# Kernel tuning notes

Hardware: AMD Instinct MI355X
Metric: run time of the kernel (lower is better)

## Reference

```python
import jax, jax.numpy as jnp
import numpy as np

DIM = 384
WS = 8        # window_size
SHIFT = 4     # shift_size
HEADS = 8
HEAD_DIM = DIM // HEADS
SCALE = HEAD_DIM ** (-0.5)
EPS = 1e-5


def layernorm(x, g, b):
    m = jnp.mean(x, axis=-1, keepdims=True)
    v = jnp.var(x, axis=-1, keepdims=True)
    return (x - m) * jax.lax.rsqrt(v + EPS) * g + b


def setup_inputs() -> dict:
    key = jax.random.key(0)
    ks = jax.random.split(key, 8)
    s = 0.02
    return {
        "x": jax.random.normal(ks[0], (8, DIM, 64, 64), dtype=jnp.float32),
        "qkv_w": jax.random.normal(ks[1], (DIM, 3 * DIM), dtype=jnp.float32) * s,
        "qkv_b": jnp.zeros((3 * DIM,), jnp.float32),
        "proj_w": jax.random.normal(ks[2], (DIM, DIM), dtype=jnp.float32) * s,
        "proj_b": jnp.zeros((DIM,), jnp.float32),
        "ln1_g": jnp.ones((DIM,), jnp.float32),
        "ln1_b": jnp.zeros((DIM,), jnp.float32),
        "ln2_g": jnp.ones((DIM,), jnp.float32),
        "ln2_b": jnp.zeros((DIM,), jnp.float32),
        "mlp_w1": jax.random.normal(ks[3], (DIM, 4 * DIM), dtype=jnp.float32) * s,
        "mlp_b1": jnp.zeros((4 * DIM,), jnp.float32),
        "mlp_w2": jax.random.normal(ks[4], (4 * DIM, DIM), dtype=jnp.float32) * s,
        "mlp_b2": jnp.zeros((DIM,), jnp.float32),
    }


def reference(x, qkv_w, qkv_b, proj_w, proj_b, ln1_g, ln1_b, ln2_g, ln2_b,
              mlp_w1, mlp_b1, mlp_w2, mlp_b2):
    B, C, H, W = x.shape
    x_skip = jnp.transpose(x, (0, 2, 3, 1))  # [B,H,W,C]
    xh = x_skip
    pad_b = (-H) % WS
    pad_r = (-W) % WS
    xh = jnp.pad(xh, ((0, 0), (0, pad_b), (0, pad_r), (0, 0)))
    Hp, Wp = xh.shape[1], xh.shape[2]
    if SHIFT > 0:
        xh = jnp.roll(xh, (-SHIFT, -SHIFT), axis=(1, 2))
    # window partition -> [B*nH*nW, WS*WS, C]
    win = xh.reshape(B, Hp // WS, WS, Wp // WS, WS, C)
    win = win.transpose(0, 1, 3, 2, 4, 5).reshape(-1, WS * WS, C)
    win = layernorm(win, ln1_g, ln1_b)
    # windowed MHA (no shift mask in original module)
    Bw, N, _ = win.shape
    qkv = (win @ qkv_w + qkv_b).reshape(Bw, N, 3, HEADS, HEAD_DIM)
    qkv = qkv.transpose(2, 0, 3, 1, 4)  # [3, Bw, H, N, d]
    q, k, v = qkv[0] * SCALE, qkv[1], qkv[2]
    attn = jax.nn.softmax(jnp.einsum('bhnd,bhmd->bhnm', q, k), axis=-1)
    out = jnp.einsum('bhnm,bhmd->bhnd', attn, v)
    out = out.transpose(0, 2, 1, 3).reshape(Bw, N, C)
    out = out @ proj_w + proj_b
    # window reverse
    xh = out.reshape(B, Hp // WS, Wp // WS, WS, WS, C)
    xh = xh.transpose(0, 1, 3, 2, 4, 5).reshape(B, Hp, Wp, C)
    if SHIFT > 0:
        xh = jnp.roll(xh, (SHIFT, SHIFT), axis=(1, 2))
    xh = xh[:, :H, :W, :] + x_skip
    h = layernorm(xh, ln2_g, ln2_b)
    h = jax.nn.gelu(h @ mlp_w1 + mlp_b1, approximate=False) @ mlp_w2 + mlp_b2
    return jnp.transpose(h, (0, 3, 1, 2))  # [B,C,H,W]
```

## Files before the change

### kernel.cpp

```cpp
#include <hip/hip_runtime.h>
#include <hip/hip_bf16.h>
#include <math.h>

#define DIM   384
#define HEADS 8
#define HD    48
#define NTOK  32768
#define NWIN  512

typedef __attribute__((ext_vector_type(8))) short bf16x8;
typedef __attribute__((ext_vector_type(8))) unsigned short u16x8;
typedef __attribute__((ext_vector_type(4))) float f32x4;

__device__ __forceinline__ float bf2f(unsigned short u) {
    unsigned int v = ((unsigned int)u) << 16;
    return __uint_as_float(v);
}
__device__ __forceinline__ unsigned short f2bf(float f) {
    __bf16 b = (__bf16)f;
    return __builtin_bit_cast(unsigned short, b);
}

__device__ __forceinline__ float gelu(float v) {
    float z  = v * 0.70710678118654752f;
    float az = fabsf(z);
    float t  = __builtin_amdgcn_rcpf(1.0f + 0.47047f * az);
    float p  = t * (0.3480242f + t * (-0.0958798f + t * 0.7478556f));
    float ea = 1.0f - p * __expf(-az * az);
    float er = copysignf(ea, z);
    return 0.5f * v * (1.0f + er);
}

__device__ __forceinline__ void tok2src(int tok, int& b, int& hs, int& ws) {
    int bb  = tok >> 12;
    int win = (tok >> 6) & 63;
    int t   = tok & 63;
    int hi = win >> 3, wi = win & 7;
    int r  = t >> 3,  cc = t & 7;
    b  = bb;
    hs = (hi * 8 + r  + 4) & 63;
    ws = (wi * 8 + cc + 4) & 63;
}

__global__ __launch_bounds__(256) void k_wt4(const float* __restrict__ qkv_w,
                                             const float* __restrict__ proj_w,
                                             const float* __restrict__ w1,
                                             const float* __restrict__ w2,
                                             unsigned short* __restrict__ d0,
                                             unsigned short* __restrict__ d1,
                                             unsigned short* __restrict__ d2,
                                             unsigned short* __restrict__ d3) {
    __shared__ unsigned short T[64][66];
    int b = blockIdx.x;
    const float* W; unsigned short* Wt; int K, N, lt;
    if (b < 108)      { W = qkv_w;  Wt = d0; K = 384;  N = 1152; lt = b; }
    else if (b < 144) { W = proj_w; Wt = d1; K = 384;  N = 384;  lt = b - 108; }
    else if (b < 288) { W = w1;     Wt = d2; K = 384;  N = 1536; lt = b - 144; }
    else              { W = w2;     Wt = d3; K = 1536; N = 384;  lt = b - 288; }
    int tn = N >> 6;
    int k0 = (lt / tn) << 6, n0 = (lt % tn) << 6;
    int t  = threadIdx.x;
    int cl = t & 63, rw = t >> 6;
    #pragma unroll
    for (int p = 0; p < 16; p++) {
        int kk = p * 4 + rw;
        T[cl][kk] = f2bf(W[(size_t)(k0 + kk) * N + n0 + cl]);
    }
    __syncthreads();
    #pragma unroll
    for (int p = 0; p < 16; p++) {
        int nn = p * 4 + rw;
        Wt[(size_t)(n0 + nn) * K + k0 + cl] = T[nn][cl];
    }
}

__global__ __launch_bounds__(256) void k_ln1(const float* __restrict__ x,
                                             const float* __restrict__ g,
                                             const float* __restrict__ bt,
                                             unsigned short* __restrict__ ln1) {
    int blk = blockIdx.x;
    int b  = blk >> 6, hs = blk & 63;
    int t  = threadIdx.x;
    int w  = t & 63, cg = t >> 6;
    const float* row = x + (size_t)b * DIM * 4096 + hs * 64;

    float v[96];
    float sum = 0.f, sq = 0.f;
    #pragma unroll
    for (int i = 0; i < 96; i++) {
        int c = i * 4 + cg;
        float xv = row[(size_t)c * 4096 + w];
        v[i] = xv;
        sum += xv; sq += xv * xv;
    }
    __shared__ float red[2][4][64];
    __shared__ float mean_s[64], rstd_s[64];
    red[0][cg][w] = sum; red[1][cg][w] = sq;
    __syncthreads();
    if (t < 64) {
        float s  = red[0][0][t] + red[0][1][t] + red[0][2][t] + red[0][3][t];
        float q2 = red[1][0][t] + red[1][1][t] + red[1][2][t] + red[1][3][t];
        float mean = s * (1.0f / DIM);
        float var  = q2 * (1.0f / DIM) - mean * mean;
        mean_s[t] = mean;
        rstd_s[t] = rsqrtf(var + 1e-5f);
    }
    __syncthreads();

    int wp = t >> 2, seg = t & 3;
    int hr = (hs + 60) & 63, wr = (wp + 60) & 63;
    int tok = ((b * 8 + (hr >> 3)) * 8 + (wr >> 3)) * 64 + (hr & 7) * 8 + (wr & 7);

    __shared__ __align__(16) unsigned short tile[64][72];
    #pragma unroll
    for (int chunk = 0; chunk < 6; chunk++) {
        float mean = mean_s[w], rstd = rstd_s[w];
        #pragma unroll
        for (int it = 0; it < 16; it++) {
            int cl = it * 4 + cg;
            int c  = chunk * 64 + cl;
            tile[w][cl] = f2bf((v[chunk * 16 + it] - mean) * rstd * g[c] + bt[c]);
        }
        __syncthreads();
        u16x8 v0 = *(const u16x8*)&tile[wp][seg * 16];
        u16x8 v1 = *(const u16x8*)&tile[wp][seg * 16 + 8];
        unsigned short* op = ln1 + (size_t)tok * DIM + chunk * 64 + seg * 16;
        *(u16x8*)op = v0;
        *(u16x8*)(op + 8) = v1;
        __syncthreads();
    }
}

template <int EPI, int K>
__global__ __launch_bounds__(256) void k_gemm_mfma(
        const unsigned short* __restrict__ A,
        const unsigned short* __restrict__ Bt,
        const float* __restrict__ bias,
        void* __restrict__ Cout,
        const float* __restrict__ xres,
        int N, int GX) {
    __shared__ __align__(16) unsigned short SH[24576];
    int tid  = threadIdx.x;
    int lane = tid & 63;
    int wave = tid >> 6;
    int wm = wave >> 1, wn = wave & 1;
    int quad = lane >> 4, l15 = lane & 15;

    int l   = blockIdx.x;
    int xcd = l & 7;
    int r_  = l >> 3;
    int bx  = r_ % GX;
    int by  = (r_ / GX) * 8 + xcd;
    int m0 = by * 128, n0 = bx * 128;

    const unsigned short* gA0 = A  + (size_t)(m0 +      lane) * K + wave * 8;
    const unsigned short* gA1 = A  + (size_t)(m0 + 64 + lane) * K + wave * 8;
    const unsigned short* gB0 = Bt + (size_t)(n0 +      lane) * K + wave * 8;
    const unsigned short* gB1 = Bt + (size_t)(n0 + 64 + lane) * K + wave * 8;

    auto stage = [&](int buf) {
        __builtin_amdgcn_global_load_lds(
            (const __attribute__((address_space(1))) void*)gA0,
            (__attribute__((address_space(3))) void*)&SH[buf * 4096 + wave * 1024],
            16, 0, 0);
        __builtin_amdgcn_global_load_lds(
            (const __attribute__((address_space(1))) void*)gA1,
            (__attribute__((address_space(3))) void*)&SH[buf * 4096 + wave * 1024 + 512],
            16, 0, 0);
        __builtin_amdgcn_global_load_lds(
            (const __attribute__((address_space(1))) void*)gB0,
            (__attribute__((address_space(3))) void*)&SH[12288 + buf * 4096 + wave * 1024],
            16, 0, 0);
        __builtin_amdgcn_global_load_lds(
            (const __attribute__((address_space(1))) void*)gB1,
            (__attribute__((address_space(3))) void*)&SH[12288 + buf * 4096 + wave * 1024 + 512],
            16, 0, 0);
        gA0 += 32; gA1 += 32; gB0 += 32; gB1 += 32;
    };

    f32x4 acc[4][4] = {};
    constexpr int NSTEPS = K >> 5;
    constexpr int U = NSTEPS / 3;

    int oa = (quad * 128 + wm * 64 + l15) * 8;
    int ob = 12288 + (quad * 128 + wn * 64 + l15) * 8;

    stage(0);
    stage(1);

#define GSTEP(CUR, NXT, MODE)                                                \
    {                                                                        \
        __builtin_amdgcn_s_barrier();                                        \
        if constexpr ((MODE) == 0) {                                         \
            stage(NXT);                                                      \
            asm volatile("s_waitcnt vmcnt(8)" ::: "memory");                 \
        } else if constexpr ((MODE) == 1) {                                  \
            asm volatile("s_waitcnt vmcnt(4)" ::: "memory");                 \
        } else {                                                             \
            asm volatile("s_waitcnt vmcnt(0)" ::: "memory");                 \
        }                                                                    \
        __builtin_amdgcn_s_barrier();                                        \
        bf16x8 af[4], bfr[4];                                                \
        _Pragma("unroll")                                                    \
        for (int r = 0; r < 4; r++)                                          \
            af[r] = *(const bf16x8*)&SH[(CUR) * 4096 + oa + r * 128];        \
        _Pragma("unroll")                                                    \
        for (int r2 = 0; r2 < 4; r2++)                                       \
            bfr[r2] = *(const bf16x8*)&SH[(CUR) * 4096 + ob + r2 * 128];     \
        _Pragma("unroll")                                                    \
        for (int r = 0; r < 4; r++)                                          \
            _Pragma("unroll")                                                \
            for (int r2 = 0; r2 < 4; r2++)                                   \
                acc[r][r2] = __builtin_amdgcn_mfma_f32_16x16x32_bf16(        \
                                 af[r], bfr[r2], acc[r][r2], 0, 0, 0);       \
    }

    #pragma unroll 1
    for (int u = 0; u < U - 1; ++u) {
        GSTEP(0, 2, 0)
        GSTEP(1, 0, 0)
        GSTEP(2, 1, 0)
    }
    GSTEP(0, 2, 0)
    GSTEP(1, 0, 1)
    GSTEP(2, 0, 2)
#undef GSTEP

    if constexpr (EPI == 3) {
        #pragma unroll
        for (int r2 = 0; r2 < 4; r2++) {
            int n = n0 + wn * 64 + r2 * 16 + l15;
            float bn = bias[n];
            #pragma unroll
            for (int r = 0; r < 4; r++) {
                #pragma unroll
                for (int reg = 0; reg < 4; reg++) {
                    int m = m0 + wm * 64 + r * 16 + quad * 4 + reg;
                    ((float*)Cout)[(size_t)m * N + n] = acc[r][r2][reg] + bn;
                }
            }
        }
    } else if constexpr (EPI == 5) {
        float* SF = (float*)SH;
        __syncthreads();
        int b   = m0 >> 12;
        int hs0 = (m0 >> 6) & 63;
        #pragma unroll
        for (int h2 = 0; h2 < 2; h2++) {
            if (wm == h2) {
                #pragma unroll
                for (int r2 = 0; r2 < 4; r2++) {
                    int c = wn * 64 + r2 * 16 + l15;
                    float bn = bias[n0 + c];
                    #pragma unroll
                    for (int r = 0; r < 4; r++) {
                        f32x4 v4;
                        #pragma unroll
                        for (int reg = 0; reg < 4; reg++)
                            v4[reg] = acc[r][r2][reg] + bn;
                        *(f32x4*)&SF[c * 68 + r * 16 + quad * 4] = v4;
                    }
                }
            }
            __syncthreads();
            #pragma unroll
            for (int i = 0; i < 8; i++) {
                int id = tid + i * 256;
                int c  = id >> 4, ch = id & 15;
                f32x4 v = *(const f32x4*)&SF[c * 68 + ch * 4];
                float* dst = (float*)Cout + ((size_t)(b * DIM + n0 + c) * 64 + hs0 + h2) * 64;
                *(f32x4*)&dst[ch * 4] = v;
            }
            __syncthreads();
        }
    } else {
        __syncthreads();
        #pragma unroll
        for (int r2 = 0; r2 < 4; r2++) {
            int col = wn * 64 + r2 * 16 + l15;
            float bn = bias[n0 + col];
            #pragma unroll
            for (int r = 0; r < 4; r++) {
                int row0 = wm * 64 + r * 16 + quad * 4;
                #pragma unroll
                for (int reg = 0; reg < 4; reg++) {
                    int row = row0 + reg;
                    float v = acc[r][r2][reg] + bn;
                    if (EPI == 1) v = gelu(v);
                    SH[(row * 136 + col) ^ (((row >> 3) & 1) << 4)] = f2bf(v);
                }
            }
        }
        __syncthreads();
        #pragma unroll
        for (int i = 0; i < 8; i++) {
            int chunk = tid + i * 256;
            int m = chunk >> 4, nc = chunk & 15;
            int idx = (m * 136 + nc * 8) ^ (((m >> 3) & 1) << 4);
            u16x8 v = *(const u16x8*)&SH[idx];
            if (EPI == 4) {
                int n = n0 + nc * 8;
                int qi  = n / 384;
                int rem = n - qi * 384;
                int hh  = rem / 48;
                int d   = rem - hh * 48;
                *(u16x8*)&((unsigned short*)Cout)[((size_t)(qi * 8 + hh) * NTOK + m0 + m) * 48 + d] = v;
            } else {
                *(u16x8*)&((unsigned short*)Cout)[(size_t)(m0 + m) * N + n0 + nc * 8] = v;
            }
        }
    }
}

__global__ __launch_bounds__(256, 1) void k_fused(
        const unsigned short* __restrict__ qkvh,
        const unsigned short* __restrict__ proj_wt,
        const float* __restrict__ proj_b,
        const float* __restrict__ x,
        const float* __restrict__ ln2_g,
        const float* __restrict__ ln2_b,
        unsigned short* __restrict__ out) {
    __shared__ __align__(16) unsigned short lds[4][8064];
    __shared__ __align__(16) unsigned short AT[64][392];
    __shared__ float red[2][4][64];
    __shared__ float mrs[2][64];
    int tid  = threadIdx.x;
    int lane = tid & 63;
    int wave = tid >> 6;
    int quad = lane >> 4, l15 = lane & 15;
    int win  = blockIdx.x;
    int tok0 = win * 64;
    unsigned short* VT = &lds[wave][0];
    unsigned short* P  = &lds[wave][3456];
    const float scale = 0.14433756729740643f;

    for (int hi = 0; hi < 2; hi++) {
        int h = wave + hi * 4;
        const unsigned short* qb = qkvh + ((size_t)(0 * 8 + h) * NTOK + tok0) * 48;
        const unsigned short* kb = qkvh + ((size_t)(1 * 8 + h) * NTOK + tok0) * 48;
        const unsigned short* vb = qkvh + ((size_t)(2 * 8 + h) * NTOK + tok0) * 48;

        #pragma unroll
        for (int i = 0; i < 6; i++) {
            u16x8 v = *(const u16x8*)&vb[lane * 48 + i * 8];
            #pragma unroll
            for (int j = 0; j < 8; j++)
                VT[(i * 8 + j) * 72 + lane] = v[j];
        }

        bf16x8 kf[4][2];
        #pragma unroll
        for (int ni = 0; ni < 4; ni++) {
            kf[ni][0] = *(const bf16x8*)&kb[(ni * 16 + l15) * 48 + quad * 8];
            bf16x8 z = {};
            if (quad < 2)
                z = *(const bf16x8*)&kb[(ni * 16 + l15) * 48 + 32 + quad * 8];
            kf[ni][1] = z;
        }

        f32x4 sacc[4][4] = {};
        #pragma unroll
        for (int mi = 0; mi < 4; mi++) {
            bf16x8 qf0 = *(const bf16x8*)&qb[(mi * 16 + l15) * 48 + quad * 8];
            bf16x8 qf1 = {};
            if (quad < 2)
                qf1 = *(const bf16x8*)&qb[(mi * 16 + l15) * 48 + 32 + quad * 8];
            #pragma unroll
            for (int ni = 0; ni < 4; ni++) {
                sacc[mi][ni] = __builtin_amdgcn_mfma_f32_16x16x32_bf16(qf0, kf[ni][0], sacc[mi][ni], 0, 0, 0);
                sacc[mi][ni] = __builtin_amdgcn_mfma_f32_16x16x32_bf16(qf1, kf[ni][1], sacc[mi][ni], 0, 0, 0);
            }
        }

        #pragma unroll
        for (int mi = 0; mi < 4; mi++) {
            #pragma unroll
            for (int reg = 0; reg < 4; reg++) {
                float s0 = sacc[mi][0][reg] * scale;
                float s1 = sacc[mi][1][reg] * scale;
                float s2 = sacc[mi][2][reg] * scale;
                float s3 = sacc[mi][3][reg] * scale;
                float mx = fmaxf(fmaxf(s0, s1), fmaxf(s2, s3));
                #pragma unroll
                for (int off = 1; off < 16; off <<= 1)
                    mx = fmaxf(mx, __shfl_xor(mx, off));
                float e0 = __expf(s0 - mx);
                float e1 = __expf(s1 - mx);
                float e2 = __expf(s2 - mx);
                float e3 = __expf(s3 - mx);
                float sm = e0 + e1 + e2 + e3;
                #pragma unroll
                for (int off = 1; off < 16; off <<= 1)
                    sm += __shfl_xor(sm, off);
                float inv = 1.0f / sm;
                int row = mi * 16 + quad * 4 + reg;
                P[row * 72 +  0 + l15] = f2bf(e0 * inv);
                P[row * 72 + 16 + l15] = f2bf(e1 * inv);
                P[row * 72 + 32 + l15] = f2bf(e2 * inv);
                P[row * 72 + 48 + l15] = f2bf(e3 * inv);
            }
        }

        bf16x8 vf[3][2];
        #pragma unroll
        for (int ni = 0; ni < 3; ni++)
            #pragma unroll
            for (int kt = 0; kt < 2; kt++)
                vf[ni][kt] = *(const bf16x8*)&VT[(ni * 16 + l15) * 72 + kt * 32 + quad * 8];

        #pragma unroll
        for (int mi = 0; mi < 4; mi++) {
            bf16x8 pf0 = *(const bf16x8*)&P[(mi * 16 + l15) * 72 + quad * 8];
            bf16x8 pf1 = *(const bf16x8*)&P[(mi * 16 + l15) * 72 + 32 + quad * 8];
            f32x4 o[3] = {};
            #pragma unroll
            for (int ni = 0; ni < 3; ni++) {
                o[ni] = __builtin_amdgcn_mfma_f32_16x16x32_bf16(pf0, vf[ni][0], o[ni], 0, 0, 0);
                o[ni] = __builtin_amdgcn_mfma_f32_16x16x32_bf16(pf1, vf[ni][1], o[ni], 0, 0, 0);
            }
            #pragma unroll
            for (int ni = 0; ni < 3; ni++)
                #pragma unroll
                for (int reg = 0; reg < 4; reg++)
                    AT[mi * 16 + quad * 4 + reg][h * HD + ni * 16 + l15] = f2bf(o[ni][reg]);
        }
    }
    __syncthreads();

    f32x4 pacc[4][6] = {};
    const unsigned short* Bw = proj_wt + (size_t)(wave * 96) * 384;
    bf16x8 bcur[6], bnxt[6];
    #pragma unroll
    for (int nj = 0; nj < 6; nj++)
        bcur[nj] = *(const bf16x8*)&Bw[(nj * 16 + l15) * 384 + quad * 8];
    #pragma unroll 1
    for (int ks = 0; ks < 12; ++ks) {
        if (ks + 1 < 12) {
            #pragma unroll
            for (int nj = 0; nj < 6; nj++)
                bnxt[nj] = *(const bf16x8*)&Bw[(nj * 16 + l15) * 384 + (ks + 1) * 32 + quad * 8];
        }
        bf16x8 a[4];
        #pragma unroll
        for (int mi = 0; mi < 4; mi++)
            a[mi] = *(const bf16x8*)&AT[mi * 16 + l15][ks * 32 + quad * 8];
        #pragma unroll
        for (int mi = 0; mi < 4; mi++)
            #pragma unroll
            for (int nj = 0; nj < 6; nj++)
                pacc[mi][nj] = __builtin_amdgcn_mfma_f32_16x16x32_bf16(
                                   a[mi], bcur[nj], pacc[mi][nj], 0, 0, 0);
        #pragma unroll
        for (int nj = 0; nj < 6; nj++) bcur[nj] = bnxt[nj];
    }

    #pragma unroll
    for (int mi = 0; mi < 4; mi++) {
        #pragma unroll
        for (int reg = 0; reg < 4; reg++) {
            int tok = tok0 + mi * 16 + quad * 4 + reg;
            int b, hs, ws_;
            tok2src(tok, b, hs, ws_);
            const float* xr = x + (((size_t)b * DIM) * 64 + hs) * 64 + ws_;
            #pragma unroll
            for (int nj = 0; nj < 6; nj++) {
                int c = wave * 96 + nj * 16 + l15;
                pacc[mi][nj][reg] += proj_b[c] + xr[(size_t)c * 4096];
            }
        }
    }

    #pragma unroll
    for (int mi = 0; mi < 4; mi++) {
        #pragma unroll
        for (int reg = 0; reg < 4; reg++) {
            float s = 0.f, q = 0.f;
            #pragma unroll
            for (int nj = 0; nj < 6; nj++) {
                float v = pacc[mi][nj][reg];
                s += v; q += v * v;
            }
            #pragma unroll
            for (int off = 1; off < 16; off <<= 1) {
                s += __shfl_xor(s, off);
                q += __shfl_xor(q, off);
            }
            if (l15 == 0) {
                int row = mi * 16 + quad * 4 + reg;
                red[0][wave][row] = s;
                red[1][wave][row] = q;
            }
        }
    }
    __syncthreads();
    if (tid < 64) {
        float s = red[0][0][tid] + red[0][1][tid] + red[0][2][tid] + red[0][3][tid];
        float q = red[1][0][tid] + red[1][1][tid] + red[1][2][tid] + red[1][3][tid];
        float mean = s * (1.0f / DIM);
        float var  = q * (1.0f / DIM) - mean * mean;
        mrs[0][tid] = mean;
        mrs[1][tid] = rsqrtf(var + 1e-5f);
    }
    __syncthreads();

    #pragma unroll
    for (int mi = 0; mi < 4; mi++) {
        #pragma unroll
        for (int nj = 0; nj < 6; nj++) {
            int c = wave * 96 + nj * 16 + l15;
            float gg = ln2_g[c], bb = ln2_b[c];
            #pragma unroll
            for (int reg = 0; reg < 4; reg++) {
                int row = mi * 16 + quad * 4 + reg;
                float v = (pacc[mi][nj][reg] - mrs[0][row]) * mrs[1][row] * gg + bb;
                AT[row][c] = f2bf(v);
            }
        }
    }
    __syncthreads();
    #pragma unroll
    for (int i = 0; i < 12; i++) {
        int id  = tid + i * 256;
        int row = id / 48, ch = id - row * 48;
        int b, hs, ws_;
        tok2src(tok0 + row, b, hs, ws_);
        int p = (b * 64 + hs) * 64 + ws_;
        u16x8 v = *(const u16x8*)&AT[row][ch * 8];
        *(u16x8*)&out[(size_t)p * DIM + ch * 8] = v;
    }
}

extern "C" void kernel_launch(void* const* d_in, const int* in_sizes, int n_in,
                              void* d_out, int out_size, void* d_ws, size_t ws_size,
                              hipStream_t stream) {
    const float* x      = (const float*)d_in[0];
    const float* qkv_w  = (const float*)d_in[1];
    const float* qkv_b  = (const float*)d_in[2];
    const float* proj_w = (const float*)d_in[3];
    const float* proj_b = (const float*)d_in[4];
    const float* ln1_g  = (const float*)d_in[5];
    const float* ln1_b  = (const float*)d_in[6];
    const float* ln2_g  = (const float*)d_in[7];
    const float* ln2_b  = (const float*)d_in[8];
    const float* w1     = (const float*)d_in[9];
    const float* b1     = (const float*)d_in[10];
    const float* w2     = (const float*)d_in[11];
    const float* b2     = (const float*)d_in[12];

    char* ws = (char*)d_ws;
    unsigned short* qkv_wt  = (unsigned short*)(ws + 0);
    unsigned short* proj_wt = (unsigned short*)(ws + 884736);
    unsigned short* w1t     = (unsigned short*)(ws + 1179648);
    unsigned short* w2t     = (unsigned short*)(ws + 2359296);
    unsigned short* ln1     = (unsigned short*)(ws + 4194304);
    unsigned short* qkv     = (unsigned short*)(ws + 29360128);
    unsigned short* ln2     = ln1;
    unsigned short* mid     = qkv;

    k_wt4<<<432, 256, 0, stream>>>(qkv_w, proj_w, w1, w2, qkv_wt, proj_wt, w1t, w2t);
    k_ln1<<<512, 256, 0, stream>>>(x, ln1_g, ln1_b, ln1);
    k_gemm_mfma<4, 384><<<9 * 256, 256, 0, stream>>>(ln1, qkv_wt, qkv_b, qkv, nullptr, 1152, 9);
    k_fused<<<NWIN, 256, 0, stream>>>(qkv, proj_wt, proj_b, x, ln2_g, ln2_b, ln2);
    k_gemm_mfma<1, 384><<<12 * 256, 256, 0, stream>>>(ln2, w1t, b1, mid, nullptr, 1536, 12);
    k_gemm_mfma<5, 1536><<<3 * 256, 256, 0, stream>>>(mid, w2t, b2, (float*)d_out, nullptr, 384, 3);
}
```

Before: 441.2 us.

## Prefetch V and residual loads, deepen proj weight prefetch, add MFMA priority

In the attention+projection kernel, the V tile for the second head is now prefetched into registers while the first head is processed. The residual x values are loaded as float4 vectors before the projection GEMM, replacing scalar strided loads after it. The proj weight prefetch is deepened to two k-steps with the loop fully unrolled, and s_setprio is raised around the MFMA blocks. The aim is to hide global memory latency behind compute, at the cost of considerably more register pressure (xres alone is 96 floats), which may reduce occupancy or cause spills.

```diff
diff --git a/kernel.cpp b/kernel.cpp
--- a/kernel.cpp
+++ b/kernel.cpp
@@ -334,18 +334,29 @@
     unsigned short* P  = &lds[wave][3456];
     const float scale = 0.14433756729740643f;
 
+    const unsigned short* vb1g = qkvh + ((size_t)(2 * 8 + wave + 4) * NTOK + tok0) * 48;
+    u16x8 vpre[6];
+    {
+        const unsigned short* vb0g = qkvh + ((size_t)(2 * 8 + wave) * NTOK + tok0) * 48;
+        #pragma unroll
+        for (int i = 0; i < 6; i++)
+            vpre[i] = *(const u16x8*)&vb0g[lane * 48 + i * 8];
+    }
+    #pragma unroll
     for (int hi = 0; hi < 2; hi++) {
         int h = wave + hi * 4;
         const unsigned short* qb = qkvh + ((size_t)(0 * 8 + h) * NTOK + tok0) * 48;
         const unsigned short* kb = qkvh + ((size_t)(1 * 8 + h) * NTOK + tok0) * 48;
-        const unsigned short* vb = qkvh + ((size_t)(2 * 8 + h) * NTOK + tok0) * 48;
-
-        #pragma unroll
-        for (int i = 0; i < 6; i++) {
-            u16x8 v = *(const u16x8*)&vb[lane * 48 + i * 8];
+
+        #pragma unroll
+        for (int i = 0; i < 6; i++)
             #pragma unroll
             for (int j = 0; j < 8; j++)
-                VT[(i * 8 + j) * 72 + lane] = v[j];
+                VT[(i * 8 + j) * 72 + lane] = vpre[i][j];
+        if (hi == 0) {
+            #pragma unroll
+            for (int i = 0; i < 6; i++)
+                vpre[i] = *(const u16x8*)&vb1g[lane * 48 + i * 8];
         }
 
         bf16x8 kf[4][2];
@@ -365,11 +376,13 @@
             bf16x8 qf1 = {};
             if (quad < 2)
                 qf1 = *(const bf16x8*)&qb[(mi * 16 + l15) * 48 + 32 + quad * 8];
+            __builtin_amdgcn_s_setprio(1);
             #pragma unroll
             for (int ni = 0; ni < 4; ni++) {
                 sacc[mi][ni] = __builtin_amdgcn_mfma_f32_16x16x32_bf16(qf0, kf[ni][0], sacc[mi][ni], 0, 0, 0);
                 sacc[mi][ni] = __builtin_amdgcn_mfma_f32_16x16x32_bf16(qf1, kf[ni][1], sacc[mi][ni], 0, 0, 0);
             }
+            __builtin_amdgcn_s_setprio(0);
         }
 
         #pragma unroll
@@ -413,11 +426,13 @@
             bf16x8 pf0 = *(const bf16x8*)&P[(mi * 16 + l15) * 72 + quad * 8];
             bf16x8 pf1 = *(const bf16x8*)&P[(mi * 16 + l15) * 72 + 32 + quad * 8];
             f32x4 o[3] = {};
+            __builtin_amdgcn_s_setprio(1);
             #pragma unroll
             for (int ni = 0; ni < 3; ni++) {
                 o[ni] = __builtin_amdgcn_mfma_f32_16x16x32_bf16(pf0, vf[ni][0], o[ni], 0, 0, 0);
                 o[ni] = __builtin_amdgcn_mfma_f32_16x16x32_bf16(pf1, vf[ni][1], o[ni], 0, 0, 0);
             }
+            __builtin_amdgcn_s_setprio(0);
             #pragma unroll
             for (int ni = 0; ni < 3; ni++)
                 #pragma unroll
@@ -427,48 +442,62 @@
     }
     __syncthreads();
 
+    int bimg = win >> 6;
+    int hi_i = (win >> 3) & 7, wi_i = win & 7;
+    int ws0  = (wi_i * 8 + ((quad & 1) << 2) + 4) & 63;
+    f32x4 xres[4][6];
+    #pragma unroll
+    for (int mi = 0; mi < 4; mi++) {
+        int hs_ = (hi_i * 8 + mi * 2 + (quad >> 1) + 4) & 63;
+        #pragma unroll
+        for (int nj = 0; nj < 6; nj++) {
+            int c = wave * 96 + nj * 16 + l15;
+            xres[mi][nj] = *(const f32x4*)&x[((size_t)(bimg * DIM + c) * 64 + hs_) * 64 + ws0];
+        }
+    }
+
     f32x4 pacc[4][6] = {};
     const unsigned short* Bw = proj_wt + (size_t)(wave * 96) * 384;
-    bf16x8 bcur[6], bnxt[6];
+    bf16x8 bk0[6], bk1[6];
     #pragma unroll
     for (int nj = 0; nj < 6; nj++)
-        bcur[nj] = *(const bf16x8*)&Bw[(nj * 16 + l15) * 384 + quad * 8];
-    #pragma unroll 1
+        bk0[nj] = *(const bf16x8*)&Bw[(nj * 16 + l15) * 384 + quad * 8];
+    #pragma unroll
+    for (int nj = 0; nj < 6; nj++)
+        bk1[nj] = *(const bf16x8*)&Bw[(nj * 16 + l15) * 384 + 32 + quad * 8];
+    #pragma unroll
     for (int ks = 0; ks < 12; ++ks) {
-        if (ks + 1 < 12) {
+        bf16x8 bk2[6] = {};
+        if (ks + 2 < 12) {
             #pragma unroll
             for (int nj = 0; nj < 6; nj++)
-                bnxt[nj] = *(const bf16x8*)&Bw[(nj * 16 + l15) * 384 + (ks + 1) * 32 + quad * 8];
+                bk2[nj] = *(const bf16x8*)&Bw[(nj * 16 + l15) * 384 + (ks + 2) * 32 + quad * 8];
         }
         bf16x8 a[4];
         #pragma unroll
         for (int mi = 0; mi < 4; mi++)
             a[mi] = *(const bf16x8*)&AT[mi * 16 + l15][ks * 32 + quad * 8];
+        __builtin_amdgcn_s_setprio(1);
         #pragma unroll
         for (int mi = 0; mi < 4; mi++)
             #pragma unroll
             for (int nj = 0; nj < 6; nj++)
                 pacc[mi][nj] = __builtin_amdgcn_mfma_f32_16x16x32_bf16(
-                                   a[mi], bcur[nj], pacc[mi][nj], 0, 0, 0);
-        #pragma unroll
-        for (int nj = 0; nj < 6; nj++) bcur[nj] = bnxt[nj];
-    }
-
-    #pragma unroll
-    for (int mi = 0; mi < 4; mi++) {
-        #pragma unroll
-        for (int reg = 0; reg < 4; reg++) {
-            int tok = tok0 + mi * 16 + quad * 4 + reg;
-            int b, hs, ws_;
-            tok2src(tok, b, hs, ws_);
-            const float* xr = x + (((size_t)b * DIM) * 64 + hs) * 64 + ws_;
-            #pragma unroll
-            for (int nj = 0; nj < 6; nj++) {
-                int c = wave * 96 + nj * 16 + l15;
-                pacc[mi][nj][reg] += proj_b[c] + xr[(size_t)c * 4096];
-            }
-        }
-    }
+                                   a[mi], bk0[nj], pacc[mi][nj], 0, 0, 0);
+        __builtin_amdgcn_s_setprio(0);
+        #pragma unroll
+        for (int nj = 0; nj < 6; nj++) { bk0[nj] = bk1[nj]; bk1[nj] = bk2[nj]; }
+    }
+
+    #pragma unroll
+    for (int mi = 0; mi < 4; mi++)
+        #pragma unroll
+        for (int nj = 0; nj < 6; nj++) {
+            float bn = proj_b[wave * 96 + nj * 16 + l15];
+            #pragma unroll
+            for (int reg = 0; reg < 4; reg++)
+                pacc[mi][nj][reg] += bn + xres[mi][nj][reg];
+        }
 
     #pragma unroll
     for (int mi = 0; mi < 4; mi++) {
```

After: 450.3 us. 1.02x slower.
